# Performance work log

Measured on AMD Instinct MI355X. Metric: run time of the kernel, lower is better.

## Reference

```python
import math
import jax, jax.numpy as jnp
import numpy as np

DIM = 1024
B, T = 4, 2048


def setup_inputs() -> dict:
    key = jax.random.key(0)
    ks = jax.random.split(key, 7)
    std = 0.02
    x = jax.random.normal(ks[0], (B, T, DIM), dtype=jnp.float32)
    Wq = jax.random.normal(ks[1], (DIM, DIM), dtype=jnp.float32) * std
    Wk = jax.random.normal(ks[2], (DIM, DIM), dtype=jnp.float32) * std
    Wv = jax.random.normal(ks[3], (DIM, DIM), dtype=jnp.float32) * std
    Wo = jax.random.normal(ks[4], (DIM, DIM), dtype=jnp.float32) * std
    # decay_proj: torch init is zero weight, bias = decay_init; use a small random
    # weight so the data-dependent decay path is exercised.
    Wd = jax.random.normal(ks[5], (1, DIM), dtype=jnp.float32) * std
    bd = jnp.full((1,), 3.0, dtype=jnp.float32)  # decay_init
    out_scale = jnp.full((1,), 0.1, dtype=jnp.float32)
    return {"x": x, "Wq": Wq, "Wk": Wk, "Wv": Wv, "Wo": Wo,
            "Wd": Wd, "bd": bd, "out_scale": out_scale}


def reference(x, Wq, Wk, Wv, Wo, Wd, bd, out_scale):
    Bsz, Tlen, dim = x.shape
    scale = 1.0 / math.sqrt(dim)
    # torch Linear: y = x @ W.T
    q = jnp.einsum('btd,ed->bte', x, Wq)
    k = jnp.einsum('btd,ed->bte', x, Wk)
    v = jnp.einsum('btd,ed->bte', x, Wv)
    scores = jnp.einsum('btd,bsd->bts', q, k) * scale            # [B,T,T]
    decay_logits = jnp.einsum('btd,ed->bte', x, Wd)[..., 0] + bd  # [B,T]
    decay = jax.nn.sigmoid(decay_logits)
    pos = jnp.arange(Tlen)
    diff = pos[None, :] - pos[:, None]                            # diff[i,j] = j - i
    causal = (diff > 0).astype(x.dtype)                           # [T,T]
    log_decay = jnp.log(decay + 1e-8)                             # [B,T]
    dist = jnp.clip(diff.astype(x.dtype) - 1.0, 0.0)              # [T,T]
    # log_weights[b,i,j] = log_decay[b,j] * dist[i,j]
    log_weights = log_decay[:, None, :] * dist[None, :, :]
    weights = jnp.exp(log_weights) * causal[None, :, :]
    scores = scores * weights
    retrieved = jnp.einsum('bts,bsd->btd', scores, v)
    out = jnp.einsum('btd,ed->bte', retrieved, Wo) * out_scale
    return out
```

## Files before the change

kernel.cpp:

```cpp
#include <hip/hip_runtime.h>


using u16 = unsigned short;
typedef __bf16 bf16x8 __attribute__((ext_vector_type(8)));
typedef float f32x4 __attribute__((ext_vector_type(4)));

__device__ inline u16 f2bf(float f) {
  unsigned u = __builtin_bit_cast(unsigned, f);
  unsigned r = (u + 0x7FFFu + ((u >> 16) & 1u)) >> 16;
  return (u16)r;
}

__device__ inline void gload16(const u16* g, u16* l) {
  __builtin_amdgcn_global_load_lds(
      (const __attribute__((address_space(1))) void*)g,
      (__attribute__((address_space(3))) void*)l, 16, 0, 0);
}

__global__ __launch_bounds__(256) void prep(const float* __restrict__ x,
    u16* __restrict__ Xbf, const float* __restrict__ Wd,
    const float* __restrict__ bd, float* __restrict__ ldec,
    const float* __restrict__ Wq, const float* __restrict__ Wk,
    const float* __restrict__ Wv, const float* __restrict__ Wo,
    u16* __restrict__ Wall) {
  int b = blockIdx.x;
  int t = threadIdx.x;
  if (b < 8192) {
    float4 f = reinterpret_cast<const float4*>(x + (size_t)b * 1024)[t];
    float4 g = reinterpret_cast<const float4*>(Wd)[t];
    ushort4 o;
    o.x = f2bf(f.x); o.y = f2bf(f.y); o.z = f2bf(f.z); o.w = f2bf(f.w);
    reinterpret_cast<ushort4*>(Xbf + (size_t)b * 1024)[t] = o;
    float s = f.x * g.x + f.y * g.y + f.z * g.z + f.w * g.w;
    #pragma unroll
    for (int off = 32; off > 0; off >>= 1) s += __shfl_xor(s, off);
    __shared__ float red[4];
    if ((t & 63) == 0) red[t >> 6] = s;
    __syncthreads();
    if (t == 0) {
      float tot = red[0] + red[1] + red[2] + red[3];
      float dec = 1.f / (1.f + expf(-(tot + bd[0])));
      ldec[b] = logf(dec + 1e-8f);
    }
  } else {
    int wb = b - 8192;
    int m = wb >> 10;
    const float* src = (m == 0) ? Wq : (m == 1) ? Wk : (m == 2) ? Wv : Wo;
    int i = ((wb & 1023) * 256 + t) * 4;
    float4 f = *reinterpret_cast<const float4*>(src + i);
    ushort4 o;
    o.x = f2bf(f.x); o.y = f2bf(f.y); o.z = f2bf(f.z); o.w = f2bf(f.w);
    *reinterpret_cast<ushort4*>(Wall + (size_t)m * 1048576 + i) = o;
  }
}

template <int EPI>
__global__ __launch_bounds__(256, 2)
void gemmP(const u16* __restrict__ Ab, const u16* __restrict__ Bb,
           void* __restrict__ Cv, int lda, int ldb, int ldc, int K,
           int tiles_n, int diag, int flip, const float* __restrict__ ldec,
           const float* __restrict__ scale_ptr,
           long long abs_, long long bbs_, long long cbs_) {
  __shared__ __align__(16) u16 lds2[32768];

  const int batch = blockIdx.y;
  const u16* A = Ab + (size_t)batch * abs_;
  const u16* B = Bb + (size_t)batch * bbs_;

  int it = blockIdx.x / tiles_n;
  const int jt = blockIdx.x % tiles_n;
  if (flip && batch >= 2) it = (gridDim.x / tiles_n - 1) - it;
  if (EPI == 1 && jt < it) return;
  const int m0 = it * 128, n0 = jt * 128;

  const int tid = threadIdx.x;
  const int lane = tid & 63;
  const int w = tid >> 6;
  const int wm = (w >> 1) * 64, wn = (w & 1) * 64;
  const int l15 = lane & 15, lhi = lane >> 4;
  const int lr8 = lane >> 3;
  const int schunk = (lane & 7) ^ lr8;

  const int kt0 = diag ? it * 2 : 0;
  const int nkt = K / 64;
  const int span = nkt - kt0;

  f32x4 acc[4][4];
  #pragma unroll
  for (int i = 0; i < 4; ++i)
    #pragma unroll
    for (int j = 0; j < 4; ++j) acc[i][j] = (f32x4)0.f;

  auto stage = [&](int kt, int buf) {
    const size_t kb = (size_t)kt * 64 + schunk * 8;
    u16* la = &lds2[buf * 16384];
    u16* lb = la + 8192;
    #pragma unroll
    for (int u = 0; u < 4; ++u)
      gload16(A + (size_t)(m0 + u * 32 + w * 8 + lr8) * lda + kb,
              la + (u * 32 + w * 8) * 64);
    #pragma unroll
    for (int u = 0; u < 4; ++u)
      gload16(B + (size_t)(n0 + u * 32 + w * 8 + lr8) * ldb + kb,
              lb + (u * 32 + w * 8) * 64);
  };

  stage(kt0, 0);
  asm volatile("s_waitcnt vmcnt(0)" ::: "memory");
  __builtin_amdgcn_s_barrier();

  for (int t = 0; t < span; ++t) {
    const int buf = t & 1;
    if (t + 1 < span) stage(kt0 + t + 1, buf ^ 1);

    const u16* baseA = &lds2[buf * 16384];
    const u16* baseB = baseA + 8192;
    bf16x8 af[4][2], bv[4][2];
    #pragma unroll
    for (int mi = 0; mi < 4; ++mi) {
      int r = wm + mi * 16 + l15;
      #pragma unroll
      for (int kk = 0; kk < 2; ++kk) {
        int s = (kk * 4 + lhi) ^ (r & 7);
        af[mi][kk] = *reinterpret_cast<const bf16x8*>(&baseA[r * 64 + s * 8]);
      }
    }
    #pragma unroll
    for (int ni = 0; ni < 4; ++ni) {
      int r = wn + ni * 16 + l15;
      #pragma unroll
      for (int kk = 0; kk < 2; ++kk) {
        int s = (kk * 4 + lhi) ^ (r & 7);
        bv[ni][kk] = *reinterpret_cast<const bf16x8*>(&baseB[r * 64 + s * 8]);
      }
    }

    __builtin_amdgcn_s_setprio(1);
    #pragma unroll
    for (int kk = 0; kk < 2; ++kk)
      #pragma unroll
      for (int mi = 0; mi < 4; ++mi)
        #pragma unroll
        for (int ni = 0; ni < 4; ++ni)
          acc[mi][ni] = __builtin_amdgcn_mfma_f32_16x16x32_bf16(
              af[mi][kk], bv[ni][kk], acc[mi][ni], 0, 0, 0);
    __builtin_amdgcn_s_setprio(0);

    asm volatile("s_waitcnt vmcnt(0)" ::: "memory");
    __builtin_amdgcn_s_barrier();
  }

  if (EPI == 0) {
    u16* C = (u16*)Cv + (size_t)batch * cbs_;
    #pragma unroll
    for (int mi = 0; mi < 4; ++mi)
      #pragma unroll
      for (int q = 0; q < 4; ++q) {
        int row = m0 + wm + mi * 16 + lhi * 4 + q;
        u16* crow = C + (size_t)row * ldc + n0 + wn + l15;
        #pragma unroll
        for (int ni = 0; ni < 4; ++ni) crow[ni * 16] = f2bf(acc[mi][ni][q]);
      }
  } else if (EPI == 1) {
    u16* C = (u16*)Cv + (size_t)batch * cbs_;
    const float* ldp = ldec + (size_t)batch * 2048;
    float ldv[4];
    #pragma unroll
    for (int ni = 0; ni < 4; ++ni) ldv[ni] = ldp[n0 + wn + ni * 16 + l15];
    const float sc = 0.03125f;
    #pragma unroll
    for (int mi = 0; mi < 4; ++mi)
      #pragma unroll
      for (int q = 0; q < 4; ++q) {
        int row = m0 + wm + mi * 16 + lhi * 4 + q;
        u16* crow = C + (size_t)row * ldc + n0 + wn + l15;
        #pragma unroll
        for (int ni = 0; ni < 4; ++ni) {
          int col = n0 + wn + ni * 16 + l15;
          int d = col - row;
          float wgt = (d > 0) ? expf(ldv[ni] * (float)(d - 1)) : 0.f;
          crow[ni * 16] = f2bf(acc[mi][ni][q] * sc * wgt);
        }
      }
  } else {
    float* C = (float*)Cv + (size_t)batch * cbs_;
    const float sc = scale_ptr[0];
    #pragma unroll
    for (int mi = 0; mi < 4; ++mi)
      #pragma unroll
      for (int q = 0; q < 4; ++q) {
        int row = m0 + wm + mi * 16 + lhi * 4 + q;
        float* crow = C + (size_t)row * ldc + n0 + wn + l15;
        #pragma unroll
        for (int ni = 0; ni < 4; ++ni) crow[ni * 16] = acc[mi][ni][q] * sc;
      }
  }
}

extern "C" void kernel_launch(void* const* d_in, const int* in_sizes, int n_in,
                              void* d_out, int out_size, void* d_ws, size_t ws_size,
                              hipStream_t stream) {
  const float* x   = (const float*)d_in[0];
  const float* Wq  = (const float*)d_in[1];
  const float* Wk  = (const float*)d_in[2];
  const float* Wv  = (const float*)d_in[3];
  const float* Wo  = (const float*)d_in[4];
  const float* Wd  = (const float*)d_in[5];
  const float* bd  = (const float*)d_in[6];
  const float* osc = (const float*)d_in[7];
  float* out = (float*)d_out;

  char* ws = (char*)d_ws;
  size_t off = 0;
  u16* Xbf  = (u16*)(ws + off); off += (size_t)8192 * 1024 * 2;
  u16* Wall = (u16*)(ws + off); off += (size_t)4096 * 1024 * 2;
  u16* VT   = (u16*)(ws + off); off += (size_t)1024 * 8192 * 2;
  u16* S    = (u16*)(ws + off); off += (size_t)4 * 2048 * 2048 * 2;
  float* ldec = (float*)(ws + off); off += (size_t)8192 * 4;
  u16* QK   = (u16*)(ws + off); off += (size_t)8192 * 2048 * 2;
  u16* R    = QK;

  u16* Wqk = Wall;
  u16* Wvb = Wall + 2 * 1048576;
  u16* Wob = Wall + 3 * 1048576;

  prep<<<12288, 256, 0, stream>>>(x, Xbf, Wd, bd, ldec, Wq, Wk, Wv, Wo, Wall);

  gemmP<0><<<dim3(64 * 16, 1), 256, 0, stream>>>(
      Xbf, Wqk, QK, 1024, 1024, 2048, 1024, 16, 0, 0, nullptr, nullptr,
      0, 0, 0);

  gemmP<0><<<dim3(8 * 64, 1), 256, 0, stream>>>(
      Wvb, Xbf, VT, 1024, 1024, 8192, 1024, 64, 0, 0, nullptr, nullptr,
      0, 0, 0);

  gemmP<1><<<dim3(16 * 16, 4), 256, 0, stream>>>(
      QK, QK + 1024, S, 2048, 2048, 2048, 1024, 16, 0, 0, ldec, nullptr,
      4194304LL, 4194304LL, 4194304LL);

  gemmP<0><<<dim3(16 * 8, 4), 256, 0, stream>>>(
      S, VT, R, 2048, 8192, 1024, 2048, 8, 1, 1, nullptr, nullptr,
      4194304LL, 2048LL, 2097152LL);

  gemmP<2><<<dim3(64 * 8, 1), 256, 0, stream>>>(
      R, Wob, out, 1024, 1024, 1024, 1024, 8, 0, 0, nullptr, osc,
      0, 0, 0);
}
```

Baseline: 164.8 us.

## Use 256x256 tiles for QK, score and PV GEMMs with split-K on PV

Adds a 256x256-tile GEMM kernel with 8x8 MFMA accumulators per wave and uses it for the QK projection, the causal score GEMM (enumerating only upper-triangular tiles) and the score-times-V GEMM. The PV GEMM splits the K range for the first row tiles into two fp32 partials, and a new reduction kernel adds them into bf16 R, to balance work across the triangular tiles. The goal is more data reuse per LDS load and fewer blocks. The cost is much higher register pressure at one block per CU, fewer blocks than CUs, an extra kernel launch, and extra fp32 partial traffic.

```diff
diff --git a/kernel.cpp b/kernel.cpp
--- a/kernel.cpp
+++ b/kernel.cpp
@@ -54,12 +54,185 @@
   }
 }
 
+__global__ __launch_bounds__(256) void radd(const float* __restrict__ p0,
+    const float* __restrict__ p1, u16* __restrict__ R) {
+  size_t i = ((size_t)blockIdx.x * 256 + threadIdx.x) * 4;
+  float4 a = *reinterpret_cast<const float4*>(p0 + i);
+  float4 b = *reinterpret_cast<const float4*>(p1 + i);
+  size_t batch = i >> 20, within = i & 1048575;
+  ushort4 o;
+  o.x = f2bf(a.x + b.x); o.y = f2bf(a.y + b.y);
+  o.z = f2bf(a.z + b.z); o.w = f2bf(a.w + b.w);
+  *reinterpret_cast<ushort4*>(R + batch * 2097152 + within) = o;
+}
+
+template <int MODE>
+__global__ __launch_bounds__(256, 1)
+void gemmB(const u16* __restrict__ Ab, const u16* __restrict__ Bb,
+           void* __restrict__ Cv, int lda, int ldb, int ldc, int K,
+           int tiles_n, const float* __restrict__ ldec,
+           float* __restrict__ aux0, float* __restrict__ aux1,
+           long long abs_, long long bbs_, long long cbs_) {
+  __shared__ __align__(16) u16 lds2[65536];
+
+  const int batch = blockIdx.y;
+  const u16* A = Ab + (size_t)batch * abs_;
+  const u16* B = Bb + (size_t)batch * bbs_;
+
+  const int bx = blockIdx.x;
+  int it, jt, kt0, kend, ks = 0; bool part = false;
+  if (MODE == 0) {
+    it = bx / tiles_n; jt = bx % tiles_n; kt0 = 0; kend = K / 64;
+  } else if (MODE == 1) {
+    int L = bx; it = 0;
+    while (L >= 8 - it) { L -= 8 - it; ++it; }
+    jt = it + L; kt0 = 0; kend = 16;
+  } else {
+    if (bx < 32) {
+      it = bx >> 3; int rm = bx & 7; jt = rm >> 1; ks = rm & 1; part = true;
+      kt0 = ks ? 16 : 4 * it; kend = ks ? 32 : 16;
+    } else {
+      int z = bx - 32; it = 4 + (z >> 2); jt = z & 3;
+      kt0 = 4 * it; kend = 32;
+    }
+  }
+  const int m0 = it * 256, n0 = jt * 256;
+
+  const int tid = threadIdx.x;
+  const int lane = tid & 63;
+  const int w = tid >> 6;
+  const int wm = w >> 1, wn = w & 1;
+  const int l15 = lane & 15, lhi = lane >> 4;
+  const int lr8 = lane >> 3;
+  const int schunk = (lane & 7) ^ lr8;
+
+  const int span = kend - kt0;
+
+  f32x4 acc[8][8];
+  #pragma unroll
+  for (int i = 0; i < 8; ++i)
+    #pragma unroll
+    for (int j = 0; j < 8; ++j) acc[i][j] = (f32x4)0.f;
+
+  auto stage = [&](int kt, int buf) {
+    const size_t kb = (size_t)kt * 64 + schunk * 8;
+    u16* la = &lds2[buf * 32768];
+    u16* lb = la + 16384;
+    #pragma unroll
+    for (int u = 0; u < 8; ++u)
+      gload16(A + (size_t)(m0 + u * 32 + w * 8 + lr8) * lda + kb,
+              la + (u * 32 + w * 8) * 64);
+    #pragma unroll
+    for (int u = 0; u < 8; ++u)
+      gload16(B + (size_t)(n0 + u * 32 + w * 8 + lr8) * ldb + kb,
+              lb + (u * 32 + w * 8) * 64);
+  };
+
+  stage(kt0, 0);
+  asm volatile("s_waitcnt vmcnt(0)" ::: "memory");
+  __builtin_amdgcn_s_barrier();
+
+  for (int t = 0; t < span; ++t) {
+    const int buf = t & 1;
+    if (t + 1 < span) stage(kt0 + t + 1, buf ^ 1);
+
+    const u16* baseA = &lds2[buf * 32768];
+    const u16* baseB = baseA + 16384;
+
+    bf16x8 bv[8][2];
+    #pragma unroll
+    for (int ni = 0; ni < 8; ++ni) {
+      int r = wn * 128 + ni * 16 + l15;
+      #pragma unroll
+      for (int kk = 0; kk < 2; ++kk) {
+        int s = (kk * 4 + lhi) ^ (r & 7);
+        bv[ni][kk] = *reinterpret_cast<const bf16x8*>(&baseB[r * 64 + s * 8]);
+      }
+    }
+    __builtin_amdgcn_s_setprio(1);
+    #pragma unroll
+    for (int mi = 0; mi < 8; ++mi) {
+      int r = wm * 128 + mi * 16 + l15;
+      int s0 = lhi ^ (r & 7), s1 = (4 + lhi) ^ (r & 7);
+      bf16x8 a0 = *reinterpret_cast<const bf16x8*>(&baseA[r * 64 + s0 * 8]);
+      bf16x8 a1 = *reinterpret_cast<const bf16x8*>(&baseA[r * 64 + s1 * 8]);
+      #pragma unroll
+      for (int ni = 0; ni < 8; ++ni)
+        acc[mi][ni] = __builtin_amdgcn_mfma_f32_16x16x32_bf16(a0, bv[ni][0], acc[mi][ni], 0, 0, 0);
+      #pragma unroll
+      for (int ni = 0; ni < 8; ++ni)
+        acc[mi][ni] = __builtin_amdgcn_mfma_f32_16x16x32_bf16(a1, bv[ni][1], acc[mi][ni], 0, 0, 0);
+    }
+    __builtin_amdgcn_s_setprio(0);
+
+    asm volatile("s_waitcnt vmcnt(0)" ::: "memory");
+    __builtin_amdgcn_s_barrier();
+  }
+
+  if (MODE == 0) {
+    u16* C = (u16*)Cv + (size_t)batch * cbs_;
+    #pragma unroll
+    for (int mi = 0; mi < 8; ++mi)
+      #pragma unroll
+      for (int q = 0; q < 4; ++q) {
+        int row = m0 + wm * 128 + mi * 16 + lhi * 4 + q;
+        u16* crow = C + (size_t)row * ldc + n0 + wn * 128 + l15;
+        #pragma unroll
+        for (int ni = 0; ni < 8; ++ni) crow[ni * 16] = f2bf(acc[mi][ni][q]);
+      }
+  } else if (MODE == 1) {
+    u16* C = (u16*)Cv + (size_t)batch * cbs_;
+    const float* ldp = ldec + (size_t)batch * 2048;
+    float ldv[8];
+    #pragma unroll
+    for (int ni = 0; ni < 8; ++ni) ldv[ni] = ldp[n0 + wn * 128 + ni * 16 + l15];
+    const float sc = 0.03125f;
+    #pragma unroll
+    for (int mi = 0; mi < 8; ++mi)
+      #pragma unroll
+      for (int q = 0; q < 4; ++q) {
+        int row = m0 + wm * 128 + mi * 16 + lhi * 4 + q;
+        u16* crow = C + (size_t)row * ldc + n0 + wn * 128 + l15;
+        #pragma unroll
+        for (int ni = 0; ni < 8; ++ni) {
+          int col = n0 + wn * 128 + ni * 16 + l15;
+          int d = col - row;
+          float wgt = (d > 0) ? expf(ldv[ni] * (float)(d - 1)) : 0.f;
+          crow[ni * 16] = f2bf(acc[mi][ni][q] * sc * wgt);
+        }
+      }
+  } else {
+    if (part) {
+      float* P = (ks ? aux1 : aux0) + (size_t)batch * 1048576;
+      #pragma unroll
+      for (int mi = 0; mi < 8; ++mi)
+        #pragma unroll
+        for (int q = 0; q < 4; ++q) {
+          int row = m0 + wm * 128 + mi * 16 + lhi * 4 + q;
+          float* crow = P + (size_t)row * 1024 + n0 + wn * 128 + l15;
+          #pragma unroll
+          for (int ni = 0; ni < 8; ++ni) crow[ni * 16] = acc[mi][ni][q];
+        }
+    } else {
+      u16* C = (u16*)Cv + (size_t)batch * cbs_;
+      #pragma unroll
+      for (int mi = 0; mi < 8; ++mi)
+        #pragma unroll
+        for (int q = 0; q < 4; ++q) {
+          int row = m0 + wm * 128 + mi * 16 + lhi * 4 + q;
+          u16* crow = C + (size_t)row * ldc + n0 + wn * 128 + l15;
+          #pragma unroll
+          for (int ni = 0; ni < 8; ++ni) crow[ni * 16] = f2bf(acc[mi][ni][q]);
+        }
+    }
+  }
+}
+
 template <int EPI>
 __global__ __launch_bounds__(256, 2)
 void gemmP(const u16* __restrict__ Ab, const u16* __restrict__ Bb,
            void* __restrict__ Cv, int lda, int ldb, int ldc, int K,
-           int tiles_n, int diag, int flip, const float* __restrict__ ldec,
-           const float* __restrict__ scale_ptr,
+           int tiles_n, const float* __restrict__ scale_ptr,
            long long abs_, long long bbs_, long long cbs_) {
   __shared__ __align__(16) u16 lds2[32768];
 
@@ -67,10 +240,8 @@
   const u16* A = Ab + (size_t)batch * abs_;
   const u16* B = Bb + (size_t)batch * bbs_;
 
-  int it = blockIdx.x / tiles_n;
+  const int it = blockIdx.x / tiles_n;
   const int jt = blockIdx.x % tiles_n;
-  if (flip && batch >= 2) it = (gridDim.x / tiles_n - 1) - it;
-  if (EPI == 1 && jt < it) return;
   const int m0 = it * 128, n0 = jt * 128;
 
   const int tid = threadIdx.x;
@@ -81,9 +252,7 @@
   const int lr8 = lane >> 3;
   const int schunk = (lane & 7) ^ lr8;
 
-  const int kt0 = diag ? it * 2 : 0;
-  const int nkt = K / 64;
-  const int span = nkt - kt0;
+  const int span = K / 64;
 
   f32x4 acc[4][4];
   #pragma unroll
@@ -105,13 +274,13 @@
               lb + (u * 32 + w * 8) * 64);
   };
 
-  stage(kt0, 0);
+  stage(0, 0);
   asm volatile("s_waitcnt vmcnt(0)" ::: "memory");
   __builtin_amdgcn_s_barrier();
 
   for (int t = 0; t < span; ++t) {
     const int buf = t & 1;
-    if (t + 1 < span) stage(kt0 + t + 1, buf ^ 1);
+    if (t + 1 < span) stage(t + 1, buf ^ 1);
 
     const u16* baseA = &lds2[buf * 16384];
     const u16* baseB = baseA + 8192;
@@ -160,27 +329,6 @@
         u16* crow = C + (size_t)row * ldc + n0 + wn + l15;
         #pragma unroll
         for (int ni = 0; ni < 4; ++ni) crow[ni * 16] = f2bf(acc[mi][ni][q]);
-      }
-  } else if (EPI == 1) {
-    u16* C = (u16*)Cv + (size_t)batch * cbs_;
-    const float* ldp = ldec + (size_t)batch * 2048;
-    float ldv[4];
-    #pragma unroll
-    for (int ni = 0; ni < 4; ++ni) ldv[ni] = ldp[n0 + wn + ni * 16 + l15];
-    const float sc = 0.03125f;
-    #pragma unroll
-    for (int mi = 0; mi < 4; ++mi)
-      #pragma unroll
-      for (int q = 0; q < 4; ++q) {
-        int row = m0 + wm + mi * 16 + lhi * 4 + q;
-        u16* crow = C + (size_t)row * ldc + n0 + wn + l15;
-        #pragma unroll
-        for (int ni = 0; ni < 4; ++ni) {
-          int col = n0 + wn + ni * 16 + l15;
-          int d = col - row;
-          float wgt = (d > 0) ? expf(ldv[ni] * (float)(d - 1)) : 0.f;
-          crow[ni * 16] = f2bf(acc[mi][ni][q] * sc * wgt);
-        }
       }
   } else {
     float* C = (float*)Cv + (size_t)batch * cbs_;
@@ -219,6 +367,8 @@
   float* ldec = (float*)(ws + off); off += (size_t)8192 * 4;
   u16* QK   = (u16*)(ws + off); off += (size_t)8192 * 2048 * 2;
   u16* R    = QK;
+  float* Rp0 = (float*)Xbf;
+  float* Rp1 = (float*)((char*)QK + 16777216);
 
   u16* Wqk = Wall;
   u16* Wvb = Wall + 2 * 1048576;
@@ -226,23 +376,23 @@
 
   prep<<<12288, 256, 0, stream>>>(x, Xbf, Wd, bd, ldec, Wq, Wk, Wv, Wo, Wall);
 
-  gemmP<0><<<dim3(64 * 16, 1), 256, 0, stream>>>(
-      Xbf, Wqk, QK, 1024, 1024, 2048, 1024, 16, 0, 0, nullptr, nullptr,
+  gemmB<0><<<dim3(32 * 8, 1), 256, 0, stream>>>(
+      Xbf, Wqk, QK, 1024, 1024, 2048, 1024, 8, nullptr, nullptr, nullptr,
       0, 0, 0);
 
   gemmP<0><<<dim3(8 * 64, 1), 256, 0, stream>>>(
-      Wvb, Xbf, VT, 1024, 1024, 8192, 1024, 64, 0, 0, nullptr, nullptr,
-      0, 0, 0);
-
-  gemmP<1><<<dim3(16 * 16, 4), 256, 0, stream>>>(
-      QK, QK + 1024, S, 2048, 2048, 2048, 1024, 16, 0, 0, ldec, nullptr,
+      Wvb, Xbf, VT, 1024, 1024, 8192, 1024, 64, nullptr, 0, 0, 0);
+
+  gemmB<1><<<dim3(36, 4), 256, 0, stream>>>(
+      QK, QK + 1024, S, 2048, 2048, 2048, 1024, 0, ldec, nullptr, nullptr,
       4194304LL, 4194304LL, 4194304LL);
 
-  gemmP<0><<<dim3(16 * 8, 4), 256, 0, stream>>>(
-      S, VT, R, 2048, 8192, 1024, 2048, 8, 1, 1, nullptr, nullptr,
+  gemmB<2><<<dim3(48, 4), 256, 0, stream>>>(
+      S, VT, R, 2048, 8192, 1024, 2048, 0, nullptr, Rp0, Rp1,
       4194304LL, 2048LL, 2097152LL);
 
+  radd<<<4096, 256, 0, stream>>>(Rp0, Rp1, R);
+
   gemmP<2><<<dim3(64 * 8, 1), 256, 0, stream>>>(
-      R, Wob, out, 1024, 1024, 1024, 1024, 8, 0, 0, nullptr, osc,
-      0, 0, 0);
-}
+      R, Wob, out, 1024, 1024, 1024, 1024, 8, osc, 0, 0, 0);
+}
```

Result: slower. 235.1 us (+42.6%).

## Switch GEMMs to 2-wave 128x128 tiles with single-buffered LDS and compact triangular grid

Applied to the files above, without the earlier changes.

Replaces the 4-wave, double-buffered GEMM with a 2-wave version. Each wave computes a 128x64 slice of the 128x128 tile, so each thread holds twice as many accumulators. LDS staging becomes single-buffered with a barrier before and after each load, so global loads no longer overlap MFMA work. The QK^T score GEMM now launches only upper-triangle tiles (136 per batch) through a linear-to-triangle index map instead of launching and early-exiting the lower blocks. The aim is less LDS traffic per MFMA and fewer wasted blocks, at the cost of lost load/compute overlap and higher register pressure.

```diff
diff --git a/kernel.cpp b/kernel.cpp
--- a/kernel.cpp
+++ b/kernel.cpp
@@ -54,129 +54,113 @@
   }
 }
 
-template <int EPI>
-__global__ __launch_bounds__(256, 2)
-void gemmP(const u16* __restrict__ Ab, const u16* __restrict__ Bb,
+template <int MODE>
+__global__ __launch_bounds__(128, 2)
+void gemmT(const u16* __restrict__ Ab, const u16* __restrict__ Bb,
            void* __restrict__ Cv, int lda, int ldb, int ldc, int K,
            int tiles_n, int diag, int flip, const float* __restrict__ ldec,
            const float* __restrict__ scale_ptr,
            long long abs_, long long bbs_, long long cbs_) {
-  __shared__ __align__(16) u16 lds2[32768];
+  __shared__ __align__(16) u16 lds[16384];
 
   const int batch = blockIdx.y;
   const u16* A = Ab + (size_t)batch * abs_;
   const u16* B = Bb + (size_t)batch * bbs_;
 
-  int it = blockIdx.x / tiles_n;
-  const int jt = blockIdx.x % tiles_n;
-  if (flip && batch >= 2) it = (gridDim.x / tiles_n - 1) - it;
-  if (EPI == 1 && jt < it) return;
+  int it, jt;
+  if (MODE == 1) {
+    int L = blockIdx.x; it = 0;
+    while (L >= 16 - it) { L -= 16 - it; ++it; }
+    jt = it + L;
+  } else {
+    it = blockIdx.x / tiles_n; jt = blockIdx.x % tiles_n;
+    if (flip && batch >= 2) it = (gridDim.x / tiles_n - 1) - it;
+  }
   const int m0 = it * 128, n0 = jt * 128;
 
   const int tid = threadIdx.x;
   const int lane = tid & 63;
   const int w = tid >> 6;
-  const int wm = (w >> 1) * 64, wn = (w & 1) * 64;
   const int l15 = lane & 15, lhi = lane >> 4;
   const int lr8 = lane >> 3;
   const int schunk = (lane & 7) ^ lr8;
 
-  const int kt0 = diag ? it * 2 : 0;
-  const int nkt = K / 64;
-  const int span = nkt - kt0;
-
-  f32x4 acc[4][4];
+  const int kt0 = (MODE != 1 && diag) ? it * 2 : 0;
+  const int span = K / 64 - kt0;
+
+  f32x4 acc[8][4];
   #pragma unroll
-  for (int i = 0; i < 4; ++i)
+  for (int i = 0; i < 8; ++i)
     #pragma unroll
     for (int j = 0; j < 4; ++j) acc[i][j] = (f32x4)0.f;
 
-  auto stage = [&](int kt, int buf) {
-    const size_t kb = (size_t)kt * 64 + schunk * 8;
-    u16* la = &lds2[buf * 16384];
-    u16* lb = la + 8192;
-    #pragma unroll
-    for (int u = 0; u < 4; ++u)
-      gload16(A + (size_t)(m0 + u * 32 + w * 8 + lr8) * lda + kb,
-              la + (u * 32 + w * 8) * 64);
-    #pragma unroll
-    for (int u = 0; u < 4; ++u)
-      gload16(B + (size_t)(n0 + u * 32 + w * 8 + lr8) * ldb + kb,
-              lb + (u * 32 + w * 8) * 64);
-  };
-
-  stage(kt0, 0);
-  asm volatile("s_waitcnt vmcnt(0)" ::: "memory");
-  __builtin_amdgcn_s_barrier();
-
   for (int t = 0; t < span; ++t) {
-    const int buf = t & 1;
-    if (t + 1 < span) stage(kt0 + t + 1, buf ^ 1);
-
-    const u16* baseA = &lds2[buf * 16384];
-    const u16* baseB = baseA + 8192;
-    bf16x8 af[4][2], bv[4][2];
-    #pragma unroll
-    for (int mi = 0; mi < 4; ++mi) {
-      int r = wm + mi * 16 + l15;
+    __syncthreads();
+    const size_t kb = (size_t)(kt0 + t) * 64 + schunk * 8;
+    #pragma unroll
+    for (int u = 0; u < 8; ++u)
+      gload16(A + (size_t)(m0 + u * 16 + w * 8 + lr8) * lda + kb,
+              &lds[(u * 16 + w * 8) * 64]);
+    #pragma unroll
+    for (int u = 0; u < 8; ++u)
+      gload16(B + (size_t)(n0 + u * 16 + w * 8 + lr8) * ldb + kb,
+              &lds[8192 + (u * 16 + w * 8) * 64]);
+    __syncthreads();
+
+    bf16x8 bv[4][2];
+    #pragma unroll
+    for (int ni = 0; ni < 4; ++ni) {
+      int r = w * 64 + ni * 16 + l15;
       #pragma unroll
       for (int kk = 0; kk < 2; ++kk) {
         int s = (kk * 4 + lhi) ^ (r & 7);
-        af[mi][kk] = *reinterpret_cast<const bf16x8*>(&baseA[r * 64 + s * 8]);
+        bv[ni][kk] = *reinterpret_cast<const bf16x8*>(&lds[8192 + r * 64 + s * 8]);
       }
     }
-    #pragma unroll
-    for (int ni = 0; ni < 4; ++ni) {
-      int r = wn + ni * 16 + l15;
-      #pragma unroll
-      for (int kk = 0; kk < 2; ++kk) {
-        int s = (kk * 4 + lhi) ^ (r & 7);
-        bv[ni][kk] = *reinterpret_cast<const bf16x8*>(&baseB[r * 64 + s * 8]);
-      }
+    __builtin_amdgcn_s_setprio(1);
+    #pragma unroll
+    for (int mi = 0; mi < 8; ++mi) {
+      int r = mi * 16 + l15;
+      int s0 = lhi ^ (r & 7), s1 = (4 + lhi) ^ (r & 7);
+      bf16x8 a0 = *reinterpret_cast<const bf16x8*>(&lds[r * 64 + s0 * 8]);
+      bf16x8 a1 = *reinterpret_cast<const bf16x8*>(&lds[r * 64 + s1 * 8]);
+      #pragma unroll
+      for (int ni = 0; ni < 4; ++ni)
+        acc[mi][ni] = __builtin_amdgcn_mfma_f32_16x16x32_bf16(a0, bv[ni][0], acc[mi][ni], 0, 0, 0);
+      #pragma unroll
+      for (int ni = 0; ni < 4; ++ni)
+        acc[mi][ni] = __builtin_amdgcn_mfma_f32_16x16x32_bf16(a1, bv[ni][1], acc[mi][ni], 0, 0, 0);
     }
-
-    __builtin_amdgcn_s_setprio(1);
-    #pragma unroll
-    for (int kk = 0; kk < 2; ++kk)
-      #pragma unroll
-      for (int mi = 0; mi < 4; ++mi)
-        #pragma unroll
-        for (int ni = 0; ni < 4; ++ni)
-          acc[mi][ni] = __builtin_amdgcn_mfma_f32_16x16x32_bf16(
-              af[mi][kk], bv[ni][kk], acc[mi][ni], 0, 0, 0);
     __builtin_amdgcn_s_setprio(0);
-
-    asm volatile("s_waitcnt vmcnt(0)" ::: "memory");
-    __builtin_amdgcn_s_barrier();
-  }
-
-  if (EPI == 0) {
+  }
+
+  if (MODE == 0) {
     u16* C = (u16*)Cv + (size_t)batch * cbs_;
     #pragma unroll
-    for (int mi = 0; mi < 4; ++mi)
+    for (int mi = 0; mi < 8; ++mi)
       #pragma unroll
       for (int q = 0; q < 4; ++q) {
-        int row = m0 + wm + mi * 16 + lhi * 4 + q;
-        u16* crow = C + (size_t)row * ldc + n0 + wn + l15;
+        int row = m0 + mi * 16 + lhi * 4 + q;
+        u16* crow = C + (size_t)row * ldc + n0 + w * 64 + l15;
         #pragma unroll
         for (int ni = 0; ni < 4; ++ni) crow[ni * 16] = f2bf(acc[mi][ni][q]);
       }
-  } else if (EPI == 1) {
+  } else if (MODE == 1) {
     u16* C = (u16*)Cv + (size_t)batch * cbs_;
     const float* ldp = ldec + (size_t)batch * 2048;
     float ldv[4];
     #pragma unroll
-    for (int ni = 0; ni < 4; ++ni) ldv[ni] = ldp[n0 + wn + ni * 16 + l15];
+    for (int ni = 0; ni < 4; ++ni) ldv[ni] = ldp[n0 + w * 64 + ni * 16 + l15];
     const float sc = 0.03125f;
     #pragma unroll
-    for (int mi = 0; mi < 4; ++mi)
+    for (int mi = 0; mi < 8; ++mi)
       #pragma unroll
       for (int q = 0; q < 4; ++q) {
-        int row = m0 + wm + mi * 16 + lhi * 4 + q;
-        u16* crow = C + (size_t)row * ldc + n0 + wn + l15;
+        int row = m0 + mi * 16 + lhi * 4 + q;
+        u16* crow = C + (size_t)row * ldc + n0 + w * 64 + l15;
         #pragma unroll
         for (int ni = 0; ni < 4; ++ni) {
-          int col = n0 + wn + ni * 16 + l15;
+          int col = n0 + w * 64 + ni * 16 + l15;
           int d = col - row;
           float wgt = (d > 0) ? expf(ldv[ni] * (float)(d - 1)) : 0.f;
           crow[ni * 16] = f2bf(acc[mi][ni][q] * sc * wgt);
@@ -186,11 +170,11 @@
     float* C = (float*)Cv + (size_t)batch * cbs_;
     const float sc = scale_ptr[0];
     #pragma unroll
-    for (int mi = 0; mi < 4; ++mi)
+    for (int mi = 0; mi < 8; ++mi)
       #pragma unroll
       for (int q = 0; q < 4; ++q) {
-        int row = m0 + wm + mi * 16 + lhi * 4 + q;
-        float* crow = C + (size_t)row * ldc + n0 + wn + l15;
+        int row = m0 + mi * 16 + lhi * 4 + q;
+        float* crow = C + (size_t)row * ldc + n0 + w * 64 + l15;
         #pragma unroll
         for (int ni = 0; ni < 4; ++ni) crow[ni * 16] = acc[mi][ni][q] * sc;
       }
@@ -226,23 +210,23 @@
 
   prep<<<12288, 256, 0, stream>>>(x, Xbf, Wd, bd, ldec, Wq, Wk, Wv, Wo, Wall);
 
-  gemmP<0><<<dim3(64 * 16, 1), 256, 0, stream>>>(
+  gemmT<0><<<dim3(64 * 16, 1), 128, 0, stream>>>(
       Xbf, Wqk, QK, 1024, 1024, 2048, 1024, 16, 0, 0, nullptr, nullptr,
       0, 0, 0);
 
-  gemmP<0><<<dim3(8 * 64, 1), 256, 0, stream>>>(
+  gemmT<0><<<dim3(8 * 64, 1), 128, 0, stream>>>(
       Wvb, Xbf, VT, 1024, 1024, 8192, 1024, 64, 0, 0, nullptr, nullptr,
       0, 0, 0);
 
-  gemmP<1><<<dim3(16 * 16, 4), 256, 0, stream>>>(
-      QK, QK + 1024, S, 2048, 2048, 2048, 1024, 16, 0, 0, ldec, nullptr,
+  gemmT<1><<<dim3(136, 4), 128, 0, stream>>>(
+      QK, QK + 1024, S, 2048, 2048, 2048, 1024, 0, 0, 0, ldec, nullptr,
       4194304LL, 4194304LL, 4194304LL);
 
-  gemmP<0><<<dim3(16 * 8, 4), 256, 0, stream>>>(
+  gemmT<0><<<dim3(16 * 8, 4), 128, 0, stream>>>(
       S, VT, R, 2048, 8192, 1024, 2048, 8, 1, 1, nullptr, nullptr,
       4194304LL, 2048LL, 2097152LL);
 
-  gemmP<2><<<dim3(64 * 8, 1), 256, 0, stream>>>(
+  gemmT<2><<<dim3(64 * 8, 1), 128, 0, stream>>>(
       R, Wob, out, 1024, 1024, 1024, 1024, 8, 0, 0, nullptr, osc,
       0, 0, 0);
 }
```

After: 202.4 us. 1.23x slower.
